# Performance work log

Hardware: AMD Instinct MI355X
Metric: run time of the kernel (lower is better)

## Reference

```python
import jax, jax.numpy as jnp
import numpy as np

S_PADDING = 65
T_PADDING = 65


def setup_inputs() -> dict:
    key = jax.random.key(0)
    k1, k2 = jax.random.split(key)
    s = jax.random.normal(k1, (32, 16, 64, 63), dtype=jnp.float32)
    t = jax.random.normal(k2, (32, 16, 64, 63), dtype=jnp.float32)
    return {"s": s, "t": t}


def reference(s, t):
    # s, t: [B, N, L, D] real. Original stacks a zero imaginary part,
    # zero-pads the D dim (dim 3 of the 5D tensor), FFTs along it,
    # then for each shift i rolls fs along N, complex-multiplies with ft,
    # concatenates along N, IFFTs, keeps real part, and permutes to [B, N*N, Dp, L].
    B, N, L, D = s.shape
    s_pad = jnp.pad(s, ((0, 0), (0, 0), (0, 0), (0, S_PADDING)))  # [B,N,L,Dp]
    t_pad = jnp.pad(t, ((0, 0), (0, 0), (0, 0), (0, T_PADDING)))
    FS = jnp.fft.fft(s_pad, axis=-1)  # complex64 [B,N,L,Dp]
    FT = jnp.fft.fft(t_pad, axis=-1)
    # roll(fs, i, axis=1)[:, n] == fs[:, (n - i) % N]; loop i is outer in the cat
    idx = (jnp.arange(N)[None, :] - jnp.arange(N)[:, None]) % N  # [i, n]
    FS_all = FS[:, idx]  # [B, N(i), N(n), L, Dp]
    Hf = FS_all * FT[:, None]  # broadcast over shift dim i
    Dp = D + S_PADDING
    Hf = Hf.reshape(B, N * N, L, Dp)
    H = jnp.fft.ifft(Hf, axis=-1).real  # [B, N*N, L, Dp]
    return H.transpose(0, 1, 3, 2)  # [B, N*N, Dp, L]
```

## Files before the change

### kernel.cpp

```cpp
#include <hip/hip_runtime.h>


#define D_IN 63
#define L_DIM 64
#define N_DIM 16
#define DP 128

__global__ __launch_bounds__(64) void conv_kernel(
    const float* __restrict__ s, const float* __restrict__ t,
    float* __restrict__ out)
{
    const int blk = blockIdx.x;
    const int b  = blk >> 8;
    const int ij = blk & 255;
    const int i  = ij >> 4;
    const int j  = ij & 15;
    const int k  = (j - i) & 15;
    const int l  = threadIdx.x;

    const float* __restrict__ srow = s + ((((size_t)b * N_DIM + k) * L_DIM + l) * D_IN);
    const float* __restrict__ trow = t + ((((size_t)b * N_DIM + j) * L_DIM + l) * D_IN);

    float sv[D_IN], tv[D_IN];
#pragma unroll
    for (int c = 0; c < D_IN; ++c) sv[c] = srow[c];
#pragma unroll
    for (int c = 0; c < D_IN; ++c) tv[c] = trow[c];

    float* __restrict__ orow = out + ((size_t)blk * (DP * L_DIM)) + l;

#pragma unroll
    for (int d0 = 0; d0 < DP; d0 += 16) {
        float acc[16];
#pragma unroll
        for (int dd = 0; dd < 16; ++dd) acc[dd] = 0.0f;

#pragma unroll
        for (int ks = 0; ks < D_IN; ++ks) {
#pragma unroll
            for (int dd = 0; dd < 16; ++dd) {
                const int kt = d0 + dd - ks;
                if (kt >= 0 && kt < D_IN)
                    acc[dd] += sv[ks] * tv[kt];
            }
        }

#pragma unroll
        for (int dd = 0; dd < 16; ++dd)
            orow[(size_t)(d0 + dd) * L_DIM] = acc[dd];
    }
}

extern "C" void kernel_launch(void* const* d_in, const int* in_sizes, int n_in,
                              void* d_out, int out_size, void* d_ws, size_t ws_size,
                              hipStream_t stream) {
    const float* s = (const float*)d_in[0];
    const float* t = (const float*)d_in[1];
    float* out = (float*)d_out;
    hipLaunchKernelGGL(conv_kernel, dim3(32 * N_DIM * N_DIM), dim3(64), 0, stream,
                       s, t, out);
}
```

Measured before the change: 313.4 us.

## Stage s and t slices in LDS with coalesced float4 loads across four waves

Each block now holds four waves that share one s slice (fixed shift index k) and four t slices, all copied into shared memory with coalesced float4 loads. Each lane then reads its row from LDS instead of making strided per-thread global reads of 63 floats. The grid is regrouped so each block covers 4 (i,j) pairs with the same k, and the output index is recomputed to match. This adds about 80KB of LDS per block, which limits occupancy, and the LDS reads with a stride of 63 may have bank conflicts.

```diff
diff --git a/kernel.cpp b/kernel.cpp
--- a/kernel.cpp
+++ b/kernel.cpp
@@ -5,29 +5,49 @@
 #define L_DIM 64
 #define N_DIM 16
 #define DP 128
+#define SLICE (L_DIM * D_IN)
 
-__global__ __launch_bounds__(64) void conv_kernel(
+__global__ __launch_bounds__(256, 2) void conv_kernel(
     const float* __restrict__ s, const float* __restrict__ t,
     float* __restrict__ out)
 {
+    __shared__ float lds_s[SLICE];
+    __shared__ float lds_t[4][SLICE];
+
+    const int tid  = threadIdx.x;
+    const int w    = tid >> 6;
+    const int lane = tid & 63;
+
     const int blk = blockIdx.x;
-    const int b  = blk >> 8;
-    const int ij = blk & 255;
-    const int i  = ij >> 4;
-    const int j  = ij & 15;
-    const int k  = (j - i) & 15;
-    const int l  = threadIdx.x;
+    const int b   = blk >> 6;
+    const int k   = (blk >> 2) & 15;
+    const int jg  = blk & 3;
+    const int j   = jg * 4 + w;
+    const int i   = (j - k) & 15;
 
-    const float* __restrict__ srow = s + ((((size_t)b * N_DIM + k) * L_DIM + l) * D_IN);
-    const float* __restrict__ trow = t + ((((size_t)b * N_DIM + j) * L_DIM + l) * D_IN);
+    {
+        const float4* __restrict__ sp =
+            (const float4*)(s + (size_t)(b * N_DIM + k) * SLICE);
+        float4* ls4 = (float4*)lds_s;
+        for (int e = tid; e < SLICE / 4; e += 256) ls4[e] = sp[e];
+#pragma unroll
+        for (int ws = 0; ws < 4; ++ws) {
+            const float4* __restrict__ tp =
+                (const float4*)(t + (size_t)(b * N_DIM + jg * 4 + ws) * SLICE);
+            float4* lt4 = (float4*)lds_t[ws];
+            for (int e = tid; e < SLICE / 4; e += 256) lt4[e] = tp[e];
+        }
+    }
+    __syncthreads();
 
     float sv[D_IN], tv[D_IN];
 #pragma unroll
-    for (int c = 0; c < D_IN; ++c) sv[c] = srow[c];
+    for (int c = 0; c < D_IN; ++c) sv[c] = lds_s[lane * D_IN + c];
 #pragma unroll
-    for (int c = 0; c < D_IN; ++c) tv[c] = trow[c];
+    for (int c = 0; c < D_IN; ++c) tv[c] = lds_t[w][lane * D_IN + c];
 
-    float* __restrict__ orow = out + ((size_t)blk * (DP * L_DIM)) + l;
+    float* __restrict__ orow =
+        out + (size_t)((b * N_DIM + i) * N_DIM + j) * (DP * L_DIM) + lane;
 
 #pragma unroll
     for (int d0 = 0; d0 < DP; d0 += 16) {
@@ -57,6 +77,6 @@
     const float* s = (const float*)d_in[0];
     const float* t = (const float*)d_in[1];
     float* out = (float*)d_out;
-    hipLaunchKernelGGL(conv_kernel, dim3(32 * N_DIM * N_DIM), dim3(64), 0, stream,
+    hipLaunchKernelGGL(conv_kernel, dim3(32 * N_DIM * 4), dim3(256), 0, stream,
                        s, t, out);
 }
```

New measurement: 333.1 us. +6.3%, slower.
